# Performance work log

Hardware: AMD Instinct MI355X
Metric: run time of the kernel (lower is better)

The kernel has to match this reference:

```python
import jax, jax.numpy as jnp
import numpy as np

N, V, J, NB = 512, 3889, 35, 20
PARENTS = np.array([0, 0, 1, 2, 3, 4, 5, 6, 7, 8, 9, 6, 11, 12, 13, 6, 15, 16, 17, 18,
                    16, 20, 21, 22, 23, 16, 25, 26, 27, 28, 29, 30, 16, 1, 1], dtype=np.int32)


def _rodrigues(theta):
    # theta: [M,3] axis-angle -> [M,3,3] rotation matrices (batch_rodrigues)
    angle = jnp.sqrt(jnp.sum(theta * theta, axis=1, keepdims=True) + 1e-8)  # [M,1]
    r = theta / angle                                                        # [M,3]
    c = jnp.cos(angle)[..., None]                                            # [M,1,1]
    s = jnp.sin(angle)[..., None]
    rr = r[:, :, None] * r[:, None, :]                                       # [M,3,3]
    z = jnp.zeros_like(r[:, 0])
    K = jnp.stack([z, -r[:, 2], r[:, 1],
                   r[:, 2], z, -r[:, 0],
                   -r[:, 1], r[:, 0], z], axis=1).reshape(-1, 3, 3)
    eye = jnp.eye(3, dtype=theta.dtype)
    return c * eye + (1.0 - c) * rr + s * K


def _make_A(R, t):
    # R: [N,3,3], t: [N,3] -> homogeneous [N,4,4]
    n = R.shape[0]
    top = jnp.concatenate([R, t[:, :, None]], axis=2)                        # [N,3,4]
    bot = jnp.broadcast_to(jnp.array([0.0, 0.0, 0.0, 1.0], R.dtype), (n, 1, 4))
    return jnp.concatenate([top, bot], axis=1)


def _global_rigid(Rs, Jp, scales, parents):
    # Rs: [N,35,3,3], Jp: [N,35,3], scales: [N,35,3] (diag scale factors)
    # diag(s_par)^-1 @ R @ diag(s) == R * s[col] / s_par[row]
    results = [_make_A(Rs[:, 0], Jp[:, 0])]
    for i in range(1, len(parents)):  # fixed 35-joint kinematic tree
        p = int(parents[i])
        j_here = Jp[:, i] - Jp[:, p]
        rot_new = Rs[:, i] * (scales[:, i][:, None, :] / scales[:, p][:, :, None])
        results.append(results[p] @ _make_A(rot_new, j_here))
    results = jnp.stack(results, axis=1)                                     # [N,35,4,4]
    new_J = results[:, :, :3, 3]
    # A = results - pad(results @ [J;0]) : subtract rest-pose bone from last column
    init_bone = jnp.einsum('njab,njb->nja', results[:, :, :, :3], Jp)        # [N,35,4]
    A = results - jnp.pad(init_bone[..., None], ((0, 0), (0, 0), (0, 0), (3, 0)))
    return new_J, A


def reference(beta, theta, betas_extra, deform_verts, trans, v_template,
              shapedirs, posedirs, J_regressor, weights, parents):
    par = np.asarray(jax.device_get(parents))
    n = beta.shape[0]
    v_shaped = v_template + deform_verts + (beta @ shapedirs).reshape(n, V, 3)
    Jp = jnp.einsum('nvc,vj->njc', v_shaped, J_regressor)                    # [N,35,3]
    Rs = _rodrigues(theta.reshape(n * J, 3)).reshape(n, J, 3, 3)
    pose_feature = (Rs[:, 1:] - jnp.eye(3, dtype=Rs.dtype)).reshape(n, 306)
    v_posed = (pose_feature @ posedirs).reshape(n, V, 3) + v_shaped
    scales = betas_extra.reshape(n, J, 3)
    _, A = _global_rigid(Rs, Jp, scales, par)
    T = jnp.einsum('vj,njab->nvab', weights, A)                              # [N,V,4,4] LBS blend
    v_h = jnp.concatenate([v_posed, jnp.ones((n, V, 1), v_posed.dtype)], axis=2)
    verts = jnp.einsum('nvab,nvb->nva', T, v_h)[..., :3] + trans[:, None, :]
    joints = jnp.einsum('nvc,vj->njc', verts, J_regressor)
    return verts, joints, Rs


def setup_inputs() -> dict:
    key = jax.random.key(0)
    ks = jax.random.split(key, 10)
    beta = 0.5 * jax.random.normal(ks[0], (N, NB), jnp.float32)
    theta = 0.2 * jax.random.normal(ks[1], (N, J * 3), jnp.float32)
    betas_extra = jnp.exp(0.1 * jax.random.normal(ks[2], (N, J * 3), jnp.float32))  # positive scales ~1
    deform_verts = 0.01 * jax.random.normal(ks[3], (N, V, 3), jnp.float32)
    trans = jax.random.normal(ks[4], (N, 3), jnp.float32)
    v_template = jax.random.normal(ks[5], (V, 3), jnp.float32)
    shapedirs = 0.01 * jax.random.normal(ks[6], (NB, V * 3), jnp.float32)
    posedirs = 0.01 * jax.random.normal(ks[7], (306, V * 3), jnp.float32)
    Jr = jax.random.uniform(ks[8], (V, J), jnp.float32)
    J_regressor = Jr / jnp.sum(Jr, axis=0, keepdims=True)   # columns sum to 1
    Wt = jax.random.uniform(ks[9], (V, J), jnp.float32)
    weights = Wt / jnp.sum(Wt, axis=1, keepdims=True)       # rows sum to 1 (skinning weights)
    return {"beta": beta, "theta": theta, "betas_extra": betas_extra,
            "deform_verts": deform_verts, "trans": trans, "v_template": v_template,
            "shapedirs": shapedirs, "posedirs": posedirs, "J_regressor": J_regressor,
            "weights": weights, "parents": jnp.asarray(PARENTS)}
```

## Files before the change

### kernel.cpp

```cpp
#include <hip/hip_runtime.h>

#define N_   512
#define V_   3889
#define V3   11667
#define J_   35
#define NB_  20
#define PF_K 306
#define KP2  352
#define KS2  11
#define EP2  11776
#define WROWS 3920

typedef __attribute__((ext_vector_type(8))) short short8;
typedef __attribute__((ext_vector_type(4))) float f32x4;

__constant__ int c_parents[J_] = {0,0,1,2,3,4,5,6,7,8,9,6,11,12,13,6,15,16,17,18,
                                  16,20,21,22,23,16,25,26,27,28,29,30,16,1,1};

static __device__ __forceinline__ unsigned short f2bf(float x) {
  union { float f; unsigned int u; } v; v.f = x;
  unsigned int r = v.u + 0x7FFF + ((v.u >> 16) & 1);
  return (unsigned short)(r >> 16);
}

#define PA_JRT 547
#define PA_WTS 245
#define PA_PD  2024
#define PA_BLOCKS (PA_JRT + PA_WTS + PA_PD)
__global__ __launch_bounds__(256) void k_prep_a(
    const float* __restrict__ Jr,  const float* __restrict__ wts,
    const float* __restrict__ pd,  const float* __restrict__ sd,
    float* __restrict__ JrT36, unsigned short* __restrict__ wtsB,
    unsigned short* __restrict__ pdT) {
  int b = blockIdx.x;
  int t = threadIdx.x;
  if (b < PA_JRT) {
    int idx = b * 256 + t;
    if (idx >= 36 * V_) return;
    int j = idx / V_, v = idx % V_;
    JrT36[idx] = (j < J_) ? Jr[v * J_ + j] : 0.f;
  } else if (b < PA_JRT + PA_WTS) {
    int bb = b - PA_JRT;
    int v   = bb * 16 + (t >> 4);
    int jk0 = (t & 15) * 4;
    unsigned short pk[4];
#pragma unroll
    for (int i = 0; i < 4; ++i) {
      int j = jk0 + i;
      float x = (v < V_ && j < J_) ? wts[(size_t)v * J_ + j] : 0.f;
      pk[i] = f2bf(x);
    }
    *(unsigned long long*)(wtsB + (size_t)v * 64 + jk0) = *(unsigned long long*)pk;
  } else {
    int pp = b - (PA_JRT + PA_WTS);
    int ec = pp % 184, o4 = pp / 184;
    int e  = ec * 64 + (t & 63);
    int oc = o4 * 4 + (t >> 6);
    int k0 = oc * 8;
    bool ev = e < V3;
    union { unsigned short u[8]; short8 s; } pk;
#pragma unroll
    for (int ii = 0; ii < 8; ++ii) {
      int k = k0 + ii;
      float x = 0.f;
      if (ev && k < PF_K)            x = pd[(size_t)k * V3 + e];
      else if (ev && k < PF_K + NB_) x = sd[(size_t)(k - PF_K) * V3 + e];
      pk.u[ii] = f2bf(x);
    }
    *(short8*)(pdT + (size_t)e * KP2 + k0) = pk.s;
  }
}

#define JRJG 9
__global__ __launch_bounds__(512) void k_jp_plus(
    const float* __restrict__ deform, const float* __restrict__ JrT36,
    const float* __restrict__ vt,     const float* __restrict__ sd,
    float* __restrict__ JpRaw, float* __restrict__ vtsdJr) {
  __shared__ float part[8][27];
  int b = blockIdx.x;
  int t = threadIdx.x;
  int lane = t & 63, w = t >> 6;
  int jg = w & 3, vh = w >> 2;
  int j0 = jg * JRJG;

  const float* s0;
  int iv0, ivn;
  if (b < N_) {
    s0 = deform + (size_t)b * V3;
    iv0 = vh * 31; ivn = vh ? 30 : 31;
  } else {
    int bb = b - N_;
    int d = bb >> 2, ch = bb & 3;
    s0 = (d == 0) ? vt : sd + (size_t)(d - 1) * V3;
    int c0 = ch * 15, cn = (ch == 3) ? 16 : 15;
    int h = cn >> 1;
    iv0 = c0 + (vh ? h : 0);
    ivn = vh ? (cn - h) : h;
  }

  float acc[JRJG][3];
#pragma unroll
  for (int jj = 0; jj < JRJG; ++jj)
#pragma unroll
    for (int cc = 0; cc < 3; ++cc) acc[jj][cc] = 0.f;

#pragma unroll 2
  for (int i = 0; i < ivn; ++i) {
    int v = (iv0 + i) * 64 + lane;
    bool ok = v < V_;
    float jr[JRJG];
#pragma unroll
    for (int jj = 0; jj < JRJG; ++jj)
      jr[jj] = ok ? JrT36[(size_t)(j0 + jj) * V_ + v] : 0.f;
    float sx = ok ? s0[3 * v + 0] : 0.f;
    float sy = ok ? s0[3 * v + 1] : 0.f;
    float sz = ok ? s0[3 * v + 2] : 0.f;
#pragma unroll
    for (int jj = 0; jj < JRJG; ++jj) {
      acc[jj][0] += jr[jj] * sx;
      acc[jj][1] += jr[jj] * sy;
      acc[jj][2] += jr[jj] * sz;
    }
  }

#pragma unroll
  for (int jj = 0; jj < JRJG; ++jj)
#pragma unroll
    for (int cc = 0; cc < 3; ++cc) {
      float v = acc[jj][cc];
#pragma unroll
      for (int off = 32; off > 0; off >>= 1)
        v += __shfl_down(v, off, 64);
      if (lane == 0) part[w][jj * 3 + cc] = v;
    }
  __syncthreads();

  if (t < 108) {
    int g = t / 27, idx = t % 27;
    int j = g * JRJG + idx / 3;
    if (j < J_) {
      float val = part[g][idx] + part[g + 4][idx];
      if (b < N_) JpRaw[b * 105 + j * 3 + idx % 3] = val;
      else atomicAdd(&vtsdJr[((b - N_) >> 2) * 105 + j * 3 + idx % 3], val);
    }
  }
}

__global__ __launch_bounds__(512) void k_jreduce5(
    const float* __restrict__ src, const float* __restrict__ JrT36,
    float* __restrict__ dst) {
  __shared__ float part[8][27];
  int t = threadIdx.x;
  int lane = t & 63;
  int w = t >> 6;
  int jg = w & 3, vh = w >> 2;
  int n = blockIdx.x;
  int j0 = jg * JRJG;
  const float* s0 = src + (size_t)n * V3;

  float acc[JRJG][3];
#pragma unroll
  for (int jj = 0; jj < JRJG; ++jj)
#pragma unroll
    for (int cc = 0; cc < 3; ++cc) acc[jj][cc] = 0.f;

  int iv0 = vh * 31;
  int ivn = vh ? 30 : 31;
#pragma unroll 2
  for (int i = 0; i < ivn; ++i) {
    int v = (iv0 + i) * 64 + lane;
    bool ok = v < V_;
    float jr[JRJG];
#pragma unroll
    for (int jj = 0; jj < JRJG; ++jj)
      jr[jj] = ok ? JrT36[(size_t)(j0 + jj) * V_ + v] : 0.f;
    float sx = ok ? s0[3 * v + 0] : 0.f;
    float sy = ok ? s0[3 * v + 1] : 0.f;
    float sz = ok ? s0[3 * v + 2] : 0.f;
#pragma unroll
    for (int jj = 0; jj < JRJG; ++jj) {
      acc[jj][0] += jr[jj] * sx;
      acc[jj][1] += jr[jj] * sy;
      acc[jj][2] += jr[jj] * sz;
    }
  }

#pragma unroll
  for (int jj = 0; jj < JRJG; ++jj)
#pragma unroll
    for (int cc = 0; cc < 3; ++cc) {
      float v = acc[jj][cc];
#pragma unroll
      for (int off = 32; off > 0; off >>= 1)
        v += __shfl_down(v, off, 64);
      if (lane == 0) part[w][jj * 3 + cc] = v;
    }
  __syncthreads();

  if (t < 108) {
    int g = t / 27, idx = t % 27;
    int j = g * JRJG + idx / 3;
    if (j < J_)
      dst[n * 105 + j * 3 + idx % 3] = part[g][idx] + part[g + 4][idx];
  }
}

__global__ __launch_bounds__(256) void k_chain_rod(
    const float* __restrict__ theta, const float* __restrict__ JpRaw,
    const float* __restrict__ vtsdJr,
    const float* __restrict__ se,    const float* __restrict__ trans,
    const float* __restrict__ beta,
    float* __restrict__ Rs_out, unsigned short* __restrict__ pfA,
    unsigned short* __restrict__ AwB) {
  __shared__ float loc[4][J_][12];
  __shared__ float res[4][J_][12];
  __shared__ float Jp_s[4][J_][3];
  int t = threadIdx.x;
  int w = t >> 6, l = t & 63;
  int n = blockIdx.x * 4 + w;
  int mt = n >> 4, m = n & 15;

  float r[9];
  if (l < J_) {
    int j = l;
    const float* th = theta + n * (J_ * 3) + j * 3;
    float t0 = th[0], t1 = th[1], t2 = th[2];
    float angle = sqrtf(t0 * t0 + t1 * t1 + t2 * t2 + 1e-8f);
    float inv = 1.0f / angle;
    float r0 = t0 * inv, r1 = t1 * inv, r2 = t2 * inv;
    float s, c;
    sincosf(angle, &s, &c);
    float omc = 1.0f - c;
    r[0] = c + omc * r0 * r0;      r[1] = omc * r0 * r1 - s * r2;  r[2] = omc * r0 * r2 + s * r1;
    r[3] = omc * r1 * r0 + s * r2; r[4] = c + omc * r1 * r1;       r[5] = omc * r1 * r2 - s * r0;
    r[6] = omc * r2 * r0 - s * r1; r[7] = omc * r2 * r1 + s * r0;  r[8] = c + omc * r2 * r2;

    float* ro = Rs_out + (size_t)n * (J_ * 9) + j * 9;
#pragma unroll
    for (int k = 0; k < 9; ++k) ro[k] = r[k];
    if (j > 0) {
#pragma unroll
      for (int kk = 0; kk < 9; ++kk) {
        int k = (j - 1) * 9 + kk;
        float v = r[kk] - ((kk == 0 || kk == 4 || kk == 8) ? 1.0f : 0.0f);
        size_t idx = ((((size_t)mt * KS2 + (k >> 5)) * 4 + ((k >> 3) & 3)) * 16 + m) * 8 + (k & 7);
        pfA[idx] = f2bf(v);
      }
    }
    const float* bn = beta + n * NB_;
#pragma unroll
    for (int cc = 0; cc < 3; ++cc) {
      int jc = j * 3 + cc;
      float val = JpRaw[n * 105 + jc] + vtsdJr[jc];
#pragma unroll
      for (int bb = 0; bb < NB_; ++bb)
        val += bn[bb] * vtsdJr[(1 + bb) * 105 + jc];
      Jp_s[w][j][cc] = val;
    }
  } else {
    unsigned short* An = AwB + (size_t)n * 16 * 64 + l;
#pragma unroll
    for (int d = 0; d < 16; ++d) An[d * 64] = 0;
    if (l < 55) {
      int k = PF_K + (l - 35);
      size_t idx = ((((size_t)mt * KS2 + (k >> 5)) * 4 + ((k >> 3) & 3)) * 16 + m) * 8 + (k & 7);
      pfA[idx] = f2bf(beta[n * NB_ + (l - 35)]);
    } else {
      for (int k = PF_K + NB_ + (l - 55); k < KP2; k += 9) {
        size_t idx = ((((size_t)mt * KS2 + (k >> 5)) * 4 + ((k >> 3) & 3)) * 16 + m) * 8 + (k & 7);
        pfA[idx] = 0;
      }
    }
  }
  __syncthreads();

  if (l < J_) {
    int j = l;
    if (j == 0) {
#pragma unroll
      for (int rr = 0; rr < 3; ++rr) {
        loc[w][0][rr * 4 + 0] = r[rr * 3 + 0];
        loc[w][0][rr * 4 + 1] = r[rr * 3 + 1];
        loc[w][0][rr * 4 + 2] = r[rr * 3 + 2];
        loc[w][0][rr * 4 + 3] = Jp_s[w][0][rr];
      }
#pragma unroll
      for (int k = 0; k < 12; ++k) res[w][0][k] = loc[w][0][k];
    } else {
      int p = c_parents[j];
      float si[3], sp[3], jh[3];
#pragma unroll
      for (int cidx = 0; cidx < 3; ++cidx) {
        si[cidx] = se[n * 105 + j * 3 + cidx];
        sp[cidx] = se[n * 105 + p * 3 + cidx];
        jh[cidx] = Jp_s[w][j][cidx] - Jp_s[w][p][cidx];
      }
#pragma unroll
      for (int rr = 0; rr < 3; ++rr) {
        float invp = 1.0f / sp[rr];
        loc[w][j][rr * 4 + 0] = r[rr * 3 + 0] * si[0] * invp;
        loc[w][j][rr * 4 + 1] = r[rr * 3 + 1] * si[1] * invp;
        loc[w][j][rr * 4 + 2] = r[rr * 3 + 2] * si[2] * invp;
        loc[w][j][rr * 4 + 3] = jh[rr];
      }
    }
  }
  __syncthreads();

  for (int i = 1; i < J_; ++i) {
    if (l < 12) {
      int p = c_parents[i];
      int rr = l >> 2, cc = l & 3;
      float acc = (cc == 3) ? res[w][p][rr * 4 + 3] : 0.f;
#pragma unroll
      for (int k = 0; k < 3; ++k)
        acc += res[w][p][rr * 4 + k] * loc[w][i][k * 4 + cc];
      res[w][i][l] = acc;
    }
    __syncthreads();
  }

  if (l < J_) {
    int j = l;
    float jx = Jp_s[w][j][0];
    float jy = Jp_s[w][j][1];
    float jz = Jp_s[w][j][2];
    unsigned short* An = AwB + (size_t)n * 16 * 64 + j;
#pragma unroll
    for (int rr = 0; rr < 3; ++rr) {
      float a0 = res[w][j][rr * 4 + 0];
      float a1 = res[w][j][rr * 4 + 1];
      float a2 = res[w][j][rr * 4 + 2];
      float a3 = res[w][j][rr * 4 + 3] - (a0 * jx + a1 * jy + a2 * jz)
               + trans[n * 3 + rr];
      An[(rr * 4 + 0) * 64] = f2bf(a0);
      An[(rr * 4 + 1) * 64] = f2bf(a1);
      An[(rr * 4 + 2) * 64] = f2bf(a2);
      An[(rr * 4 + 3) * 64] = f2bf(a3);
    }
  }
}

#define LSTR 242
__global__ __launch_bounds__(256) void k_vposed_skin(
    const unsigned short* __restrict__ pfA, const unsigned short* __restrict__ pdT,
    const unsigned short* __restrict__ AwB, const unsigned short* __restrict__ wtsB,
    const float* __restrict__ vt, const float* __restrict__ deform,
    float* __restrict__ verts) {
  __shared__ float lds[64 * LSTR];
  int t = threadIdx.x;
  int wv = t >> 6, lane = t & 63;
  int q = lane >> 4, col = lane & 15;
  int bx = blockIdx.x, by = blockIdx.y;
  int mtg0 = by * 4;
  int ebase = bx * 240 + wv * 64;

  const short8* Ap = (const short8*)pfA;
  const short8* Bp = (const short8*)pdT;

  f32x4 acc[4][4];
#pragma unroll
  for (int mt = 0; mt < 4; ++mt)
#pragma unroll
    for (int et = 0; et < 4; ++et) acc[mt][et] = (f32x4){0.f, 0.f, 0.f, 0.f};

#pragma unroll
  for (int ks = 0; ks < KS2; ++ks) {
    short8 a[4];
#pragma unroll
    for (int mt = 0; mt < 4; ++mt)
      a[mt] = Ap[(((mtg0 + mt) * KS2 + ks) * 4 + q) * 16 + col];
    short8 b[4];
#pragma unroll
    for (int et = 0; et < 4; ++et)
      b[et] = Bp[(size_t)(ebase + et * 16 + col) * (KP2 / 8) + ks * 4 + q];
#pragma unroll
    for (int mt = 0; mt < 4; ++mt)
#pragma unroll
      for (int et = 0; et < 4; ++et)
        acc[mt][et] = __builtin_amdgcn_mfma_f32_16x16x32_bf16(a[mt], b[et], acc[mt][et], 0, 0, 0);
  }

#pragma unroll
  for (int et = 0; et < 4; ++et) {
    int e_loc = wv * 64 + et * 16 + col;
    int e = bx * 240 + e_loc;
    bool ev = (e < V3) && (e_loc < 240);
    float vte = ev ? vt[e] : 0.f;
#pragma unroll
    for (int mt = 0; mt < 4; ++mt) {
#pragma unroll
      for (int r = 0; r < 4; ++r) {
        int n_loc = mt * 16 + q * 4 + r;
        if (ev) {
          int n = by * 64 + n_loc;
          float df = deform[(size_t)n * V3 + e];
          lds[n_loc * LSTR + e_loc] = acc[mt][et][r] + vte + df;
        }
      }
    }
  }
  __syncthreads();

  short8 bw0[5], bw1[5];
#pragma unroll
  for (int v5 = 0; v5 < 5; ++v5) {
    int v = bx * 80 + v5 * 16 + col;
    const short8* Wp = (const short8*)(wtsB + (size_t)v * 64);
    bw0[v5] = Wp[q];
    bw1[v5] = Wp[4 + q];
  }
#pragma unroll 2
  for (int ni = 0; ni < 16; ++ni) {
    int n_loc = wv * 16 + ni;
    int n = by * 64 + n_loc;
    const short8* Aq = (const short8*)(AwB + ((size_t)n * 16 + col) * 64);
    short8 a0 = Aq[q];
    short8 a1 = Aq[4 + q];
#pragma unroll
    for (int v5 = 0; v5 < 5; ++v5) {
      f32x4 s = (f32x4){0.f, 0.f, 0.f, 0.f};
      s = __builtin_amdgcn_mfma_f32_16x16x32_bf16(a0, bw0[v5], s, 0, 0, 0);
      s = __builtin_amdgcn_mfma_f32_16x16x32_bf16(a1, bw1[v5], s, 0, 0, 0);
      int vl = v5 * 16 + col;
      int v = bx * 80 + vl;
      if (v < V_ && q < 3) {
        float x = lds[n_loc * LSTR + 3 * vl + 0];
        float y = lds[n_loc * LSTR + 3 * vl + 1];
        float z = lds[n_loc * LSTR + 3 * vl + 2];
        verts[(size_t)n * V3 + 3 * v + q] = s[0] * x + s[1] * y + s[2] * z + s[3];
      }
    }
  }
}

extern "C" void kernel_launch(void* const* d_in, const int* in_sizes, int n_in,
                              void* d_out, int out_size, void* d_ws, size_t ws_size,
                              hipStream_t stream) {
  const float* beta   = (const float*)d_in[0];
  const float* theta  = (const float*)d_in[1];
  const float* se     = (const float*)d_in[2];
  const float* deform = (const float*)d_in[3];
  const float* trans  = (const float*)d_in[4];
  const float* vt     = (const float*)d_in[5];
  const float* sd     = (const float*)d_in[6];
  const float* pd     = (const float*)d_in[7];
  const float* Jr     = (const float*)d_in[8];
  const float* wts    = (const float*)d_in[9];

  float* out    = (float*)d_out;
  float* verts  = out;
  float* joints = out + (size_t)N_ * V3;
  float* Rs     = joints + (size_t)N_ * 105;

  char* w = (char*)d_ws;
  unsigned short* pdT    = (unsigned short*)w;
  unsigned short* pfA    = (unsigned short*)(w + 8290304);
  float* JpRaw  = (float*)(w + 8650752);
  unsigned short* AwB    = (unsigned short*)(w + 8865792);
  float* JrT36  = (float*)(w + 9914368);
  unsigned short* wtsB   = (unsigned short*)(w + 10474384);
  float* vtsdJr = (float*)(w + 10976144);

  hipMemsetAsync(vtsdJr, 0, 21 * 105 * sizeof(float), stream);
  k_prep_a<<<PA_BLOCKS, 256, 0, stream>>>(Jr, wts, pd, sd, JrT36, wtsB, pdT);
  k_jp_plus<<<N_ + 84, 512, 0, stream>>>(deform, JrT36, vt, sd, JpRaw, vtsdJr);
  k_chain_rod<<<N_ / 4, 256, 0, stream>>>(theta, JpRaw, vtsdJr, se, trans, beta,
                                          Rs, pfA, AwB);
  k_vposed_skin<<<dim3(49, 8), 256, 0, stream>>>(pfA, pdT, AwB, wtsB, vt, deform, verts);
  k_jreduce5<<<N_, 512, 0, stream>>>(verts, JrT36, joints);
}
```

Measured before the change: 226.0 us.

## Compute joint regressions with bf16 MFMA GEMM and fold memset into prep kernel

Replaces the per-sample FP32 scalar joint-regressor reductions (for deform and final verts) with a bf16 MFMA 16x16x32 GEMM over a pre-packed Jr layout, splitting work by 16-sample tile and coordinate across 96 blocks. The vtsdJr zeroing memset moves into the prep kernel to drop a separate launch. This cuts scalar FMA work and per-sample repeated Jr loads, but uses fewer blocks with strided gathers of source data. It also lowers the regression inputs to bf16, which may hurt accuracy of joints.

```diff
diff --git a/kernel.cpp b/kernel.cpp
--- a/kernel.cpp
+++ b/kernel.cpp
@@ -10,6 +10,7 @@
 #define KS2  11
 #define EP2  11776
 #define WROWS 3920
+#define VKS 122
 
 typedef __attribute__((ext_vector_type(8))) short short8;
 typedef __attribute__((ext_vector_type(4))) float f32x4;
@@ -26,12 +27,15 @@
 #define PA_JRT 547
 #define PA_WTS 245
 #define PA_PD  2024
-#define PA_BLOCKS (PA_JRT + PA_WTS + PA_PD)
+#define PA_JRB 92
+#define PA_Z   9
+#define PA_BLOCKS (PA_JRT + PA_WTS + PA_PD + PA_JRB + PA_Z)
 __global__ __launch_bounds__(256) void k_prep_a(
     const float* __restrict__ Jr,  const float* __restrict__ wts,
     const float* __restrict__ pd,  const float* __restrict__ sd,
     float* __restrict__ JrT36, unsigned short* __restrict__ wtsB,
-    unsigned short* __restrict__ pdT) {
+    unsigned short* __restrict__ pdT, unsigned short* __restrict__ JrB,
+    float* __restrict__ vtsdJr) {
   int b = blockIdx.x;
   int t = threadIdx.x;
   if (b < PA_JRT) {
@@ -51,7 +55,7 @@
       pk[i] = f2bf(x);
     }
     *(unsigned long long*)(wtsB + (size_t)v * 64 + jk0) = *(unsigned long long*)pk;
-  } else {
+  } else if (b < PA_JRT + PA_WTS + PA_PD) {
     int pp = b - (PA_JRT + PA_WTS);
     int ec = pp % 184, o4 = pp / 184;
     int e  = ec * 64 + (t & 63);
@@ -68,141 +72,141 @@
       pk.u[ii] = f2bf(x);
     }
     *(short8*)(pdT + (size_t)e * KP2 + k0) = pk.s;
-  }
-}
-
-#define JRJG 9
-__global__ __launch_bounds__(512) void k_jp_plus(
-    const float* __restrict__ deform, const float* __restrict__ JrT36,
-    const float* __restrict__ vt,     const float* __restrict__ sd,
+  } else if (b < PA_JRT + PA_WTS + PA_PD + PA_JRB) {
+    int idx = (b - PA_JRT - PA_WTS - PA_PD) * 256 + t;
+    if (idx >= 3 * VKS * 4 * 16) return;
+    int col = idx & 15;
+    int q   = (idx >> 4) & 3;
+    int ks  = (idx >> 6) % VKS;
+    int jt  = (idx >> 6) / VKS;
+    int j = jt * 16 + col;
+    union { unsigned short u[8]; short8 s; } pk;
+#pragma unroll
+    for (int o = 0; o < 8; ++o) {
+      int v = ks * 32 + q * 8 + o;
+      float x = (v < V_ && j < J_) ? Jr[(size_t)v * J_ + j] : 0.f;
+      pk.u[o] = f2bf(x);
+    }
+    *(short8*)(JrB + (size_t)idx * 8) = pk.s;
+  } else {
+    int idx = (b - PA_JRT - PA_WTS - PA_PD - PA_JRB) * 256 + t;
+    if (idx < 21 * 105) vtsdJr[idx] = 0.f;
+  }
+}
+
+static __device__ __forceinline__ void jr_gemm(
+    const float* __restrict__ src, const unsigned short* __restrict__ JrB,
+    float* __restrict__ dst, int mt, int c, int t) {
+  __shared__ float part[4][3][64][4];
+  int wv = t >> 6, lane = t & 63;
+  int q = lane >> 4, col = lane & 15;
+  int n = mt * 16 + col;
+  const float* s0 = src + (size_t)n * V3 + c;
+  int ks0 = wv * 31;
+  int ksn = (wv == 3) ? (VKS - 93) : 31;
+  const short8* Bp = (const short8*)JrB;
+
+  f32x4 acc[3];
+#pragma unroll
+  for (int jt = 0; jt < 3; ++jt) acc[jt] = (f32x4){0.f, 0.f, 0.f, 0.f};
+
+#pragma unroll 2
+  for (int i = 0; i < ksn; ++i) {
+    int ks = ks0 + i;
+    int v0 = ks * 32 + q * 8;
+    union { unsigned short u[8]; short8 s; } a;
+#pragma unroll
+    for (int o = 0; o < 8; ++o) {
+      int v = v0 + o;
+      float x = (v < V_) ? s0[3 * v] : 0.f;
+      a.u[o] = f2bf(x);
+    }
+#pragma unroll
+    for (int jt = 0; jt < 3; ++jt) {
+      short8 bfr = Bp[((jt * VKS + ks) * 4 + q) * 16 + col];
+      acc[jt] = __builtin_amdgcn_mfma_f32_16x16x32_bf16(a.s, bfr, acc[jt], 0, 0, 0);
+    }
+  }
+#pragma unroll
+  for (int jt = 0; jt < 3; ++jt)
+#pragma unroll
+    for (int r = 0; r < 4; ++r) part[wv][jt][lane][r] = acc[jt][r];
+  __syncthreads();
+  if (t < 192) {
+    int jt = t / 64, l2 = t % 64;
+    int q2 = l2 >> 4, col2 = l2 & 15;
+    int j = jt * 16 + col2;
+    if (j < J_) {
+#pragma unroll
+      for (int r = 0; r < 4; ++r) {
+        float s = part[0][jt][l2][r] + part[1][jt][l2][r]
+                + part[2][jt][l2][r] + part[3][jt][l2][r];
+        int nn = mt * 16 + q2 * 4 + r;
+        dst[(size_t)nn * 105 + j * 3 + c] = s;
+      }
+    }
+  }
+}
+
+__global__ __launch_bounds__(256) void k_jp3(
+    const float* __restrict__ deform, const unsigned short* __restrict__ JrB,
+    const float* __restrict__ JrT36,
+    const float* __restrict__ vt, const float* __restrict__ sd,
     float* __restrict__ JpRaw, float* __restrict__ vtsdJr) {
-  __shared__ float part[8][27];
   int b = blockIdx.x;
   int t = threadIdx.x;
-  int lane = t & 63, w = t >> 6;
-  int jg = w & 3, vh = w >> 2;
-  int j0 = jg * JRJG;
-
-  const float* s0;
-  int iv0, ivn;
-  if (b < N_) {
-    s0 = deform + (size_t)b * V3;
-    iv0 = vh * 31; ivn = vh ? 30 : 31;
+  if (b < 96) {
+    jr_gemm(deform, JrB, JpRaw, b & 31, b >> 5, t);
   } else {
-    int bb = b - N_;
+    int bb = b - 96;
     int d = bb >> 2, ch = bb & 3;
-    s0 = (d == 0) ? vt : sd + (size_t)(d - 1) * V3;
+    const float* s0 = (d == 0) ? vt : sd + (size_t)(d - 1) * V3;
+    int lane = t & 63, jg = t >> 6;
+    int j0 = jg * 9;
     int c0 = ch * 15, cn = (ch == 3) ? 16 : 15;
-    int h = cn >> 1;
-    iv0 = c0 + (vh ? h : 0);
-    ivn = vh ? (cn - h) : h;
-  }
-
-  float acc[JRJG][3];
-#pragma unroll
-  for (int jj = 0; jj < JRJG; ++jj)
-#pragma unroll
-    for (int cc = 0; cc < 3; ++cc) acc[jj][cc] = 0.f;
-
+    float acc[9][3];
+#pragma unroll
+    for (int jj = 0; jj < 9; ++jj)
+#pragma unroll
+      for (int cc = 0; cc < 3; ++cc) acc[jj][cc] = 0.f;
 #pragma unroll 2
-  for (int i = 0; i < ivn; ++i) {
-    int v = (iv0 + i) * 64 + lane;
-    bool ok = v < V_;
-    float jr[JRJG];
-#pragma unroll
-    for (int jj = 0; jj < JRJG; ++jj)
-      jr[jj] = ok ? JrT36[(size_t)(j0 + jj) * V_ + v] : 0.f;
-    float sx = ok ? s0[3 * v + 0] : 0.f;
-    float sy = ok ? s0[3 * v + 1] : 0.f;
-    float sz = ok ? s0[3 * v + 2] : 0.f;
-#pragma unroll
-    for (int jj = 0; jj < JRJG; ++jj) {
-      acc[jj][0] += jr[jj] * sx;
-      acc[jj][1] += jr[jj] * sy;
-      acc[jj][2] += jr[jj] * sz;
-    }
-  }
-
-#pragma unroll
-  for (int jj = 0; jj < JRJG; ++jj)
-#pragma unroll
-    for (int cc = 0; cc < 3; ++cc) {
-      float v = acc[jj][cc];
-#pragma unroll
-      for (int off = 32; off > 0; off >>= 1)
-        v += __shfl_down(v, off, 64);
-      if (lane == 0) part[w][jj * 3 + cc] = v;
-    }
-  __syncthreads();
-
-  if (t < 108) {
-    int g = t / 27, idx = t % 27;
-    int j = g * JRJG + idx / 3;
-    if (j < J_) {
-      float val = part[g][idx] + part[g + 4][idx];
-      if (b < N_) JpRaw[b * 105 + j * 3 + idx % 3] = val;
-      else atomicAdd(&vtsdJr[((b - N_) >> 2) * 105 + j * 3 + idx % 3], val);
-    }
-  }
-}
-
-__global__ __launch_bounds__(512) void k_jreduce5(
-    const float* __restrict__ src, const float* __restrict__ JrT36,
-    float* __restrict__ dst) {
-  __shared__ float part[8][27];
-  int t = threadIdx.x;
-  int lane = t & 63;
-  int w = t >> 6;
-  int jg = w & 3, vh = w >> 2;
-  int n = blockIdx.x;
-  int j0 = jg * JRJG;
-  const float* s0 = src + (size_t)n * V3;
-
-  float acc[JRJG][3];
-#pragma unroll
-  for (int jj = 0; jj < JRJG; ++jj)
-#pragma unroll
-    for (int cc = 0; cc < 3; ++cc) acc[jj][cc] = 0.f;
-
-  int iv0 = vh * 31;
-  int ivn = vh ? 30 : 31;
-#pragma unroll 2
-  for (int i = 0; i < ivn; ++i) {
-    int v = (iv0 + i) * 64 + lane;
-    bool ok = v < V_;
-    float jr[JRJG];
-#pragma unroll
-    for (int jj = 0; jj < JRJG; ++jj)
-      jr[jj] = ok ? JrT36[(size_t)(j0 + jj) * V_ + v] : 0.f;
-    float sx = ok ? s0[3 * v + 0] : 0.f;
-    float sy = ok ? s0[3 * v + 1] : 0.f;
-    float sz = ok ? s0[3 * v + 2] : 0.f;
-#pragma unroll
-    for (int jj = 0; jj < JRJG; ++jj) {
-      acc[jj][0] += jr[jj] * sx;
-      acc[jj][1] += jr[jj] * sy;
-      acc[jj][2] += jr[jj] * sz;
-    }
-  }
-
-#pragma unroll
-  for (int jj = 0; jj < JRJG; ++jj)
-#pragma unroll
-    for (int cc = 0; cc < 3; ++cc) {
-      float v = acc[jj][cc];
-#pragma unroll
-      for (int off = 32; off > 0; off >>= 1)
-        v += __shfl_down(v, off, 64);
-      if (lane == 0) part[w][jj * 3 + cc] = v;
-    }
-  __syncthreads();
-
-  if (t < 108) {
-    int g = t / 27, idx = t % 27;
-    int j = g * JRJG + idx / 3;
-    if (j < J_)
-      dst[n * 105 + j * 3 + idx % 3] = part[g][idx] + part[g + 4][idx];
-  }
+    for (int i = 0; i < cn; ++i) {
+      int v = (c0 + i) * 64 + lane;
+      bool ok = v < V_;
+      float jr[9];
+#pragma unroll
+      for (int jj = 0; jj < 9; ++jj)
+        jr[jj] = ok ? JrT36[(size_t)(j0 + jj) * V_ + v] : 0.f;
+      float sx = ok ? s0[3 * v + 0] : 0.f;
+      float sy = ok ? s0[3 * v + 1] : 0.f;
+      float sz = ok ? s0[3 * v + 2] : 0.f;
+#pragma unroll
+      for (int jj = 0; jj < 9; ++jj) {
+        acc[jj][0] += jr[jj] * sx;
+        acc[jj][1] += jr[jj] * sy;
+        acc[jj][2] += jr[jj] * sz;
+      }
+    }
+#pragma unroll
+    for (int jj = 0; jj < 9; ++jj)
+#pragma unroll
+      for (int cc = 0; cc < 3; ++cc) {
+        float v = acc[jj][cc];
+#pragma unroll
+        for (int off = 32; off > 0; off >>= 1)
+          v += __shfl_down(v, off, 64);
+        if (lane == 0) {
+          int j = j0 + jj;
+          if (j < J_) atomicAdd(&vtsdJr[d * 105 + j * 3 + cc], v);
+        }
+      }
+  }
+}
+
+__global__ __launch_bounds__(256) void k_joints(
+    const float* __restrict__ verts, const unsigned short* __restrict__ JrB,
+    float* __restrict__ joints) {
+  jr_gemm(verts, JrB, joints, blockIdx.x & 31, blockIdx.x >> 5, threadIdx.x);
 }
 
 __global__ __launch_bounds__(256) void k_chain_rod(
@@ -461,12 +465,13 @@
   float* JrT36  = (float*)(w + 9914368);
   unsigned short* wtsB   = (unsigned short*)(w + 10474384);
   float* vtsdJr = (float*)(w + 10976144);
-
-  hipMemsetAsync(vtsdJr, 0, 21 * 105 * sizeof(float), stream);
-  k_prep_a<<<PA_BLOCKS, 256, 0, stream>>>(Jr, wts, pd, sd, JrT36, wtsB, pdT);
-  k_jp_plus<<<N_ + 84, 512, 0, stream>>>(deform, JrT36, vt, sd, JpRaw, vtsdJr);
+  unsigned short* JrB    = (unsigned short*)(w + 10985216);
+
+  k_prep_a<<<PA_BLOCKS, 256, 0, stream>>>(Jr, wts, pd, sd,
+                                          JrT36, wtsB, pdT, JrB, vtsdJr);
+  k_jp3<<<96 + 84, 256, 0, stream>>>(deform, JrB, JrT36, vt, sd, JpRaw, vtsdJr);
   k_chain_rod<<<N_ / 4, 256, 0, stream>>>(theta, JpRaw, vtsdJr, se, trans, beta,
                                           Rs, pfA, AwB);
   k_vposed_skin<<<dim3(49, 8), 256, 0, stream>>>(pfA, pdT, AwB, wtsB, vt, deform, verts);
-  k_jreduce5<<<N_, 512, 0, stream>>>(verts, JrT36, joints);
-}
+  k_joints<<<96, 256, 0, stream>>>(verts, JrB, joints);
+}
```

After: 234.0 us. +3.5%, slower.
